# Performance work log

Hardware: AMD Instinct MI355X
Metric: run time of the kernel (lower is better)

## Reference

```python
import jax, jax.numpy as jnp
import numpy as np
import math

N = 16384
IN_F = 256
OUT_F = 64
EPS = 1e-6


def setup_inputs() -> dict:
    key = jax.random.key(0)
    k1, k2, k3, k4 = jax.random.split(key, 4)
    stdv = 1.0 / math.sqrt(OUT_F)
    inp = jax.random.normal(k1, (N, IN_F), dtype=jnp.float32)
    adj = jax.random.uniform(k2, (N, N), dtype=jnp.float32)
    weight = jax.random.uniform(k3, (IN_F, OUT_F), dtype=jnp.float32, minval=-stdv, maxval=stdv)
    bias = jax.random.uniform(k4, (OUT_F,), dtype=jnp.float32, minval=-stdv, maxval=stdv)
    return {"input": inp, "adj": adj, "weight": weight, "bias": bias, "p": 2}


def reference(input, adj, weight, bias, p):
    # support: [N, OUT_F]
    support = input @ weight
    mu = jnp.min(support)  # global scalar min
    pre_sup = support - mu + EPS  # >= EPS, safe for pow
    pre_top = pre_sup ** (p + 1)
    pre_down = pre_sup ** p
    # p-power mean aggregation: two adj matmuls sharing adj reads
    output = (adj @ pre_top) / (adj @ pre_down) + mu
    return output + bias
```

## Files before the change

### kernel.cpp

```cpp
#include <hip/hip_runtime.h>
#include <hip/hip_bf16.h>

typedef __attribute__((ext_vector_type(8))) short short8;
typedef __attribute__((ext_vector_type(4))) float f32x4;
typedef unsigned short u16;
typedef unsigned int u32;

#define NROWS 16384
#define KDIM 16384
#define EPS 1e-6f

__device__ __forceinline__ u16 f2bf(float x) {
    union { float f; u32 u; } v; v.f = x;
    u32 u = v.u;
    u32 r = (u + 0x7FFFu + ((u >> 16) & 1u)) >> 16;
    return (u16)r;
}

__device__ __forceinline__ void glds16(const void* g, void* l) {
    __builtin_amdgcn_global_load_lds(
        (const __attribute__((address_space(1))) void*)g,
        (__attribute__((address_space(3))) void*)l, 16, 0, 0);
}

__device__ __forceinline__ short cvbf(float x) {
    __hip_bfloat16 h = __float2bfloat16(x);
    return *(short*)&h;
}

__device__ __forceinline__ short8 cvt8(float4 a, float4 b) {
    short8 r = { cvbf(a.x), cvbf(a.y), cvbf(a.z), cvbf(a.w),
                 cvbf(b.x), cvbf(b.y), cvbf(b.z), cvbf(b.w) };
    return r;
}

__global__ __launch_bounds__(256) void wt_kernel(const float* __restrict__ W,
                                                 float* __restrict__ Wt) {
    int idx = blockIdx.x * 256 + threadIdx.x;
    int k = idx >> 6, c = idx & 63;
    Wt[c * 256 + k] = W[idx];
}

__global__ __launch_bounds__(256) void support_kernel(
    const float* __restrict__ inp, const float* __restrict__ Wt,
    float* __restrict__ sup)
{
    int tid = threadIdx.x;
    int col = tid & 63;
    int rr = tid >> 6;
    int rowbase = blockIdx.x * 32 + rr * 8;
    const float4* wt4 = (const float4*)(Wt + (size_t)col * 256);
    float acc[8];
#pragma unroll
    for (int i = 0; i < 8; ++i) acc[i] = 0.f;
    for (int k4 = 0; k4 < 64; ++k4) {
        float4 wv = wt4[k4];
#pragma unroll
        for (int i = 0; i < 8; ++i) {
            float4 iv = *((const float4*)(inp + (size_t)(rowbase + i) * 256) + k4);
            acc[i] += iv.x * wv.x + iv.y * wv.y + iv.z * wv.z + iv.w * wv.w;
        }
    }
#pragma unroll
    for (int i = 0; i < 8; ++i)
        sup[(size_t)(rowbase + i) * 64 + col] = acc[i];
}

__global__ __launch_bounds__(256) void min_part_kernel(
    const float* __restrict__ sup, float* __restrict__ partmin)
{
    __shared__ float wmin[4];
    int tid = threadIdx.x;
    const float4* s4 = (const float4*)sup;
    size_t idx = (size_t)blockIdx.x * 256 + tid;
    float m = 3.4e38f;
#pragma unroll
    for (int j = 0; j < 4; ++j) {
        float4 v = s4[idx + (size_t)j * 65536];
        m = fminf(m, fminf(fminf(v.x, v.y), fminf(v.z, v.w)));
    }
#pragma unroll
    for (int off = 32; off; off >>= 1) m = fminf(m, __shfl_down(m, off, 64));
    if ((tid & 63) == 0) wmin[tid >> 6] = m;
    __syncthreads();
    if (tid == 0)
        partmin[blockIdx.x] = fminf(fminf(wmin[0], wmin[1]), fminf(wmin[2], wmin[3]));
}

__global__ __launch_bounds__(256) void min_final_kernel(
    const float* __restrict__ partmin, float* __restrict__ mu)
{
    __shared__ float wmin[4];
    int tid = threadIdx.x;
    float m = partmin[tid];
#pragma unroll
    for (int off = 32; off; off >>= 1) m = fminf(m, __shfl_down(m, off, 64));
    if ((tid & 63) == 0) wmin[tid >> 6] = m;
    __syncthreads();
    if (tid == 0)
        mu[0] = fminf(fminf(wmin[0], wmin[1]), fminf(wmin[2], wmin[3]));
}

__global__ __launch_bounds__(256) void build_bt_kernel(
    const float* __restrict__ sup, const float* __restrict__ muptr,
    const int* __restrict__ pptr, u16* __restrict__ Bt)
{
    int k = blockIdx.x * 256 + threadIdx.x;
    float mu = *muptr;
    int p = *pptr;
    const float4* srow = (const float4*)(sup + (size_t)k * 64);
#pragma unroll
    for (int j = 0; j < 16; ++j) {
        float4 v = srow[j];
        float ss[4] = {v.x, v.y, v.z, v.w};
#pragma unroll
        for (int q = 0; q < 4; ++q) {
            int c = j * 4 + q;
            float s = ss[q] - mu + EPS;
            float d = 1.f;
            for (int i = 0; i < p; ++i) d *= s;
            Bt[(size_t)c * KDIM + k] = f2bf(d * s);
            Bt[(size_t)(c + 64) * KDIM + k] = f2bf(d);
        }
    }
}

#define BM 64
#define BN 128
#define BK 64
#define KH 8192
#define NTI 128

__global__ __launch_bounds__(512, 4) void gemm_kernel(
    const float* __restrict__ adj, const u16* __restrict__ Bt,
    float* __restrict__ Pp)
{
    __shared__ __align__(16) float Ash[2][BM * BK];
    __shared__ __align__(16) u16  Bsh[2][BN * BK];

    const int tid = threadIdx.x;
    const int rb = blockIdx.x >> 1;
    const int h  = blockIdx.x & 1;
    const size_t rowbase = (size_t)rb * BM;
    const size_t kbase = (size_t)h * KH;

    const int ga0 = tid,        ga1 = tid + 512;
    const int ar0 = ga0 >> 4,   ax0 = (ga0 & 15) ^ (ar0 & 7);
    const int ar1 = ga1 >> 4,   ax1 = (ga1 & 15) ^ (ar1 & 7);
    const float* asrc0 = adj + (rowbase + ar0) * KDIM + kbase + ax0 * 4;
    const float* asrc1 = adj + (rowbase + ar1) * KDIM + kbase + ax1 * 4;
    const int bn0 = ga0 >> 3,   bx0 = (ga0 & 7) ^ (bn0 & 7);
    const int bn1 = ga1 >> 3,   bx1 = (ga1 & 7) ^ (bn1 & 7);
    const u16* bsrc0 = Bt + (size_t)bn0 * KDIM + kbase + bx0 * 8;
    const u16* bsrc1 = Bt + (size_t)bn1 * KDIM + kbase + bx1 * 8;

    const int lane = tid & 63;
    const int w    = tid >> 6;
    const int wm   = w >> 1;
    const int wn   = w & 1;
    const int l15  = lane & 15, lg = lane >> 4;
    const int arow = wm * 16 + l15;
    const int asw  = arow & 7;

    f32x4 acc[4];
#pragma unroll
    for (int j = 0; j < 4; ++j) acc[j] = (f32x4){0.f, 0.f, 0.f, 0.f};

    auto stage = [&](int kt, int buf) {
        const int koff = kt * BK;
        char* ab = (char*)Ash[buf];
        char* bb = (char*)Bsh[buf];
        glds16(asrc0 + koff, ab + ga0 * 16);
        glds16(asrc1 + koff, ab + ga1 * 16);
        glds16(bsrc0 + koff, bb + ga0 * 16);
        glds16(bsrc1 + koff, bb + ga1 * 16);
    };

    stage(0, 0);

    for (int t = 0; t < NTI; ++t) {
        __syncthreads();
        if (t + 1 < NTI) stage(t + 1, (t + 1) & 1);
        const float4* As4 = (const float4*)Ash[t & 1];
        const short8* Bs8 = (const short8*)Bsh[t & 1];
#pragma unroll
        for (int ks = 0; ks < 2; ++ks) {
            const int x0 = ks * 8 + lg * 2;
            float4 fa = As4[arow * 16 + ((x0    ) ^ asw)];
            float4 fb = As4[arow * 16 + ((x0 + 1) ^ asw)];
            short8 a = cvt8(fa, fb);
            const int bx = ks * 4 + lg;
#pragma unroll
            for (int j = 0; j < 4; ++j) {
                const int n = wn * 32 + (j & 1) * 16 + (j >> 1) * 64 + l15;
                short8 b = Bs8[n * 8 + (bx ^ (n & 7))];
                acc[j] = __builtin_amdgcn_mfma_f32_16x16x32_bf16(a, b, acc[j], 0, 0, 0);
            }
        }
    }

    float* pb = Pp + (size_t)blockIdx.x * (BM * BN);
#pragma unroll
    for (int j = 0; j < 2; ++j) {
#pragma unroll
        for (int q = 0; q < 4; ++q) {
            int r = wm * 16 + lg * 4 + q;
            int c = wn * 32 + j * 16 + l15;
            pb[r * BN + c]      = acc[j][q];
            pb[r * BN + c + 64] = acc[j + 2][q];
        }
    }
}

__global__ __launch_bounds__(256) void reduce_kernel(
    const float* __restrict__ Pp, const float* __restrict__ bias,
    const float* __restrict__ muptr, float* __restrict__ out)
{
    int idx = blockIdx.x * 256 + threadIdx.x;
    int r = idx >> 6, c = idx & 63;
    int rb = r >> 6, rr = r & 63;
    const float* p0 = Pp + (size_t)(rb * 2) * (BM * BN) + rr * BN + c;
    const float* p1 = p0 + BM * BN;
    float T = p0[0]  + p1[0];
    float D = p0[64] + p1[64];
    out[idx] = T / D + muptr[0] + bias[c];
}

extern "C" void kernel_launch(void* const* d_in, const int* in_sizes, int n_in,
                              void* d_out, int out_size, void* d_ws, size_t ws_size,
                              hipStream_t stream)
{
    const float* inp  = (const float*)d_in[0];
    const float* adj  = (const float*)d_in[1];
    const float* W    = (const float*)d_in[2];
    const float* bias = (const float*)d_in[3];
    const int*   p    = (const int*)d_in[4];
    float* out = (float*)d_out;

    char* ws = (char*)d_ws;
    u16*   Bt      = (u16*)ws;
    float* partmin = (float*)(ws + (size_t)4 * 1024 * 1024);
    float* mu      = partmin + 256;
    float* Wt      = (float*)(ws + (size_t)4 * 1024 * 1024 + 4096);
    float* Pp      = (float*)(ws + (size_t)8 * 1024 * 1024);

    float* sup = out;

    wt_kernel       <<<64,   256, 0, stream>>>(W, Wt);
    support_kernel  <<<512,  256, 0, stream>>>(inp, Wt, sup);
    min_part_kernel <<<256,  256, 0, stream>>>(sup, partmin);
    min_final_kernel<<<1,    256, 0, stream>>>(partmin, mu);
    build_bt_kernel <<<64,   256, 0, stream>>>(sup, mu, p, Bt);
    gemm_kernel     <<<512,  512, 0, stream>>>(adj, Bt, Pp);
    reduce_kernel   <<<4096, 256, 0, stream>>>(Pp, bias, mu, out);
}
```

Before: 290.9 us.

## Convert adj to bf16 in registers before LDS, remap blocks and warp tiling

The adj tile is now loaded into registers, converted to bf16 once per element, and stored into LDS as bf16, in place of being copied as fp32 via global_load_lds and converted per MFMA read. This halves the LDS footprint and bandwidth for A and removes redundant conversions. The warp layout changes to a 2x4 grid, with each warp computing a 2x2 set of 16x16 tiles that reuse A and B fragments. The block index is remapped so the two K-halves and neighbouring row blocks are spread across XCDs, and the partial-sum layout in the reduce kernel is updated to match. The tradeoff is that A loads now go through VGPRs, which adds register pressure and wait latency.

```diff
diff --git a/kernel.cpp b/kernel.cpp
--- a/kernel.cpp
+++ b/kernel.cpp
@@ -26,12 +26,6 @@
 __device__ __forceinline__ short cvbf(float x) {
     __hip_bfloat16 h = __float2bfloat16(x);
     return *(short*)&h;
-}
-
-__device__ __forceinline__ short8 cvt8(float4 a, float4 b) {
-    short8 r = { cvbf(a.x), cvbf(a.y), cvbf(a.z), cvbf(a.w),
-                 cvbf(b.x), cvbf(b.y), cvbf(b.z), cvbf(b.w) };
-    return r;
 }
 
 __global__ __launch_bounds__(256) void wt_kernel(const float* __restrict__ W,
@@ -135,80 +129,101 @@
     const float* __restrict__ adj, const u16* __restrict__ Bt,
     float* __restrict__ Pp)
 {
-    __shared__ __align__(16) float Ash[2][BM * BK];
-    __shared__ __align__(16) u16  Bsh[2][BN * BK];
+    __shared__ __align__(16) u16 Ash[2][BM * BK];
+    __shared__ __align__(16) u16 Bsh[2][BN * BK];
 
     const int tid = threadIdx.x;
-    const int rb = blockIdx.x >> 1;
-    const int h  = blockIdx.x & 1;
+    const int P = blockIdx.x;
+    const int L = (P & 7) * 64 + (P >> 3);
+    const int h  = L >> 8;
+    const int rb = L & 255;
     const size_t rowbase = (size_t)rb * BM;
-    const size_t kbase = (size_t)h * KH;
-
-    const int ga0 = tid,        ga1 = tid + 512;
-    const int ar0 = ga0 >> 4,   ax0 = (ga0 & 15) ^ (ar0 & 7);
-    const int ar1 = ga1 >> 4,   ax1 = (ga1 & 15) ^ (ar1 & 7);
-    const float* asrc0 = adj + (rowbase + ar0) * KDIM + kbase + ax0 * 4;
-    const float* asrc1 = adj + (rowbase + ar1) * KDIM + kbase + ax1 * 4;
-    const int bn0 = ga0 >> 3,   bx0 = (ga0 & 7) ^ (bn0 & 7);
-    const int bn1 = ga1 >> 3,   bx1 = (ga1 & 7) ^ (bn1 & 7);
+    const size_t kbase   = (size_t)h * KH;
+
+    const int ars = tid >> 3;
+    const int ac8 = tid & 7;
+    const float* asrc = adj + (rowbase + ars) * KDIM + kbase + ac8 * 8;
+    const int awoff = ars * 8 + (ac8 ^ (ars & 7));
+
+    const int ga0 = tid, ga1 = tid + 512;
+    const int bn0 = ga0 >> 3, bx0 = (ga0 & 7) ^ (bn0 & 7);
+    const int bn1 = ga1 >> 3, bx1 = (ga1 & 7) ^ (bn1 & 7);
     const u16* bsrc0 = Bt + (size_t)bn0 * KDIM + kbase + bx0 * 8;
     const u16* bsrc1 = Bt + (size_t)bn1 * KDIM + kbase + bx1 * 8;
 
     const int lane = tid & 63;
     const int w    = tid >> 6;
-    const int wm   = w >> 1;
-    const int wn   = w & 1;
+    const int wm   = w >> 2;
+    const int wn   = w & 3;
     const int l15  = lane & 15, lg = lane >> 4;
-    const int arow = wm * 16 + l15;
-    const int asw  = arow & 7;
-
-    f32x4 acc[4];
-#pragma unroll
-    for (int j = 0; j < 4; ++j) acc[j] = (f32x4){0.f, 0.f, 0.f, 0.f};
-
-    auto stage = [&](int kt, int buf) {
+    const int arow0 = wm * 32 + l15;
+    const int arow1 = arow0 + 16;
+    const int nt = wn * 16 + l15;
+    const int nd = nt + 64;
+    const int asw = arow0 & 7;
+    const int bsw = nt & 7;
+
+    f32x4 acc00 = {0.f, 0.f, 0.f, 0.f};
+    f32x4 acc01 = acc00, acc10 = acc00, acc11 = acc00;
+
+    float4 ra0, ra1;
+
+    auto issueA = [&](int kt) {
+        const float4* ap = (const float4*)(asrc + kt * BK);
+        ra0 = ap[0]; ra1 = ap[1];
+    };
+    auto issueB = [&](int kt, int buf) {
+        char* bb = (char*)Bsh[buf];
         const int koff = kt * BK;
-        char* ab = (char*)Ash[buf];
-        char* bb = (char*)Bsh[buf];
-        glds16(asrc0 + koff, ab + ga0 * 16);
-        glds16(asrc1 + koff, ab + ga1 * 16);
         glds16(bsrc0 + koff, bb + ga0 * 16);
         glds16(bsrc1 + koff, bb + ga1 * 16);
     };
-
-    stage(0, 0);
+    auto writeA = [&](int buf) {
+        uint4 awv;
+        awv.x = (u32)(u16)cvbf(ra0.x) | ((u32)(u16)cvbf(ra0.y) << 16);
+        awv.y = (u32)(u16)cvbf(ra0.z) | ((u32)(u16)cvbf(ra0.w) << 16);
+        awv.z = (u32)(u16)cvbf(ra1.x) | ((u32)(u16)cvbf(ra1.y) << 16);
+        awv.w = (u32)(u16)cvbf(ra1.z) | ((u32)(u16)cvbf(ra1.w) << 16);
+        ((uint4*)Ash[buf])[awoff] = awv;
+    };
+
+    issueA(0);
+    issueB(0, 0);
+    writeA(0);
 
     for (int t = 0; t < NTI; ++t) {
         __syncthreads();
-        if (t + 1 < NTI) stage(t + 1, (t + 1) & 1);
-        const float4* As4 = (const float4*)Ash[t & 1];
+        const int nb = (t + 1) & 1;
+        if (t + 1 < NTI) {
+            issueA(t + 1);
+            issueB(t + 1, nb);
+        }
+        const short8* As8 = (const short8*)Ash[t & 1];
         const short8* Bs8 = (const short8*)Bsh[t & 1];
 #pragma unroll
         for (int ks = 0; ks < 2; ++ks) {
-            const int x0 = ks * 8 + lg * 2;
-            float4 fa = As4[arow * 16 + ((x0    ) ^ asw)];
-            float4 fb = As4[arow * 16 + ((x0 + 1) ^ asw)];
-            short8 a = cvt8(fa, fb);
-            const int bx = ks * 4 + lg;
-#pragma unroll
-            for (int j = 0; j < 4; ++j) {
-                const int n = wn * 32 + (j & 1) * 16 + (j >> 1) * 64 + l15;
-                short8 b = Bs8[n * 8 + (bx ^ (n & 7))];
-                acc[j] = __builtin_amdgcn_mfma_f32_16x16x32_bf16(a, b, acc[j], 0, 0, 0);
-            }
-        }
-    }
-
-    float* pb = Pp + (size_t)blockIdx.x * (BM * BN);
-#pragma unroll
-    for (int j = 0; j < 2; ++j) {
-#pragma unroll
-        for (int q = 0; q < 4; ++q) {
-            int r = wm * 16 + lg * 4 + q;
-            int c = wn * 32 + j * 16 + l15;
-            pb[r * BN + c]      = acc[j][q];
-            pb[r * BN + c + 64] = acc[j + 2][q];
-        }
+            const int g = ks * 4 + lg;
+            short8 a0 = As8[arow0 * 8 + (g ^ asw)];
+            short8 a1 = As8[arow1 * 8 + (g ^ asw)];
+            short8 b0 = Bs8[nt * 8 + (g ^ bsw)];
+            short8 b1 = Bs8[nd * 8 + (g ^ bsw)];
+            acc00 = __builtin_amdgcn_mfma_f32_16x16x32_bf16(a0, b0, acc00, 0, 0, 0);
+            acc01 = __builtin_amdgcn_mfma_f32_16x16x32_bf16(a0, b1, acc01, 0, 0, 0);
+            acc10 = __builtin_amdgcn_mfma_f32_16x16x32_bf16(a1, b0, acc10, 0, 0, 0);
+            acc11 = __builtin_amdgcn_mfma_f32_16x16x32_bf16(a1, b1, acc11, 0, 0, 0);
+        }
+        if (t + 1 < NTI) writeA(nb);
+    }
+
+    float* pb = Pp + (size_t)L * (BM * BN);
+#pragma unroll
+    for (int q = 0; q < 4; ++q) {
+        int r0 = wm * 32 + lg * 4 + q;
+        int r1 = r0 + 16;
+        pb[r0 * BN + nt] = acc00[q];
+        pb[r0 * BN + nd] = acc01[q];
+        pb[r1 * BN + nt] = acc10[q];
+        pb[r1 * BN + nd] = acc11[q];
     }
 }
 
@@ -219,8 +234,8 @@
     int idx = blockIdx.x * 256 + threadIdx.x;
     int r = idx >> 6, c = idx & 63;
     int rb = r >> 6, rr = r & 63;
-    const float* p0 = Pp + (size_t)(rb * 2) * (BM * BN) + rr * BN + c;
-    const float* p1 = p0 + BM * BN;
+    const float* p0 = Pp + (size_t)rb * (BM * BN) + rr * BN + c;
+    const float* p1 = p0 + (size_t)256 * (BM * BN);
     float T = p0[0]  + p1[0];
     float D = p0[64] + p1[64];
     out[idx] = T / D + muptr[0] + bias[c];
```

Result: slower. 327.2 us (+12.5%).

## Shrink GEMM tile to 32 rows and 32-wide K with 256-thread blocks

Applied to the files above, without the earlier changes.

Halves the GEMM block tile in M (64 to 32 rows) and in K step (64 to 32), uses 256 threads per block and launches 1024 blocks instead of 512. The load mapping, LDS swizzle, MFMA inner loop and reduce indexing are rewritten to match. The aim is more blocks and waves for better CU occupancy and latency hiding on the memory-bound adj stream. In exchange, each block re-reads the B tile for fewer output rows and does twice as many barrier iterations.

```diff
diff --git a/kernel.cpp b/kernel.cpp
--- a/kernel.cpp
+++ b/kernel.cpp
@@ -125,13 +125,13 @@
     }
 }
 
-#define BM 64
+#define BM 32
 #define BN 128
-#define BK 64
+#define BK 32
 #define KH 8192
-#define NTI 128
-
-__global__ __launch_bounds__(512, 4) void gemm_kernel(
+#define NTI 256
+
+__global__ __launch_bounds__(256, 4) void gemm_kernel(
     const float* __restrict__ adj, const u16* __restrict__ Bt,
     float* __restrict__ Pp)
 {
@@ -142,15 +142,15 @@
     const int rb = blockIdx.x >> 1;
     const int h  = blockIdx.x & 1;
     const size_t rowbase = (size_t)rb * BM;
-    const size_t kbase = (size_t)h * KH;
-
-    const int ga0 = tid,        ga1 = tid + 512;
-    const int ar0 = ga0 >> 4,   ax0 = (ga0 & 15) ^ (ar0 & 7);
-    const int ar1 = ga1 >> 4,   ax1 = (ga1 & 15) ^ (ar1 & 7);
-    const float* asrc0 = adj + (rowbase + ar0) * KDIM + kbase + ax0 * 4;
-    const float* asrc1 = adj + (rowbase + ar1) * KDIM + kbase + ax1 * 4;
-    const int bn0 = ga0 >> 3,   bx0 = (ga0 & 7) ^ (bn0 & 7);
-    const int bn1 = ga1 >> 3,   bx1 = (ga1 & 7) ^ (bn1 & 7);
+    const size_t kbase   = (size_t)h * KH;
+
+    const int ar = tid >> 3;
+    const int ax = (tid & 7) ^ (ar & 7);
+    const float* asrc = adj + (rowbase + ar) * KDIM + kbase + ax * 4;
+
+    const int g0 = tid, g1 = tid + 256;
+    const int bn0 = g0 >> 2, bx0 = (g0 & 3) ^ (bn0 & 3);
+    const int bn1 = g1 >> 2, bx1 = (g1 & 3) ^ (bn1 & 3);
     const u16* bsrc0 = Bt + (size_t)bn0 * KDIM + kbase + bx0 * 8;
     const u16* bsrc1 = Bt + (size_t)bn1 * KDIM + kbase + bx1 * 8;
 
@@ -159,21 +159,22 @@
     const int wm   = w >> 1;
     const int wn   = w & 1;
     const int l15  = lane & 15, lg = lane >> 4;
-    const int arow = wm * 16 + l15;
-    const int asw  = arow & 7;
-
-    f32x4 acc[4];
-#pragma unroll
-    for (int j = 0; j < 4; ++j) acc[j] = (f32x4){0.f, 0.f, 0.f, 0.f};
+    const int ar0  = wm * 16 + l15;
+    const int asw  = ar0 & 7;
+    const int n0   = wn * 32 + l15;
+    const int n1   = n0 + 16;
+    const int bs0  = n0 & 3, bs1 = n1 & 3;
+
+    f32x4 acc0 = {0.f, 0.f, 0.f, 0.f};
+    f32x4 acc1 = acc0, acc2 = acc0, acc3 = acc0;
 
     auto stage = [&](int kt, int buf) {
         const int koff = kt * BK;
         char* ab = (char*)Ash[buf];
         char* bb = (char*)Bsh[buf];
-        glds16(asrc0 + koff, ab + ga0 * 16);
-        glds16(asrc1 + koff, ab + ga1 * 16);
-        glds16(bsrc0 + koff, bb + ga0 * 16);
-        glds16(bsrc1 + koff, bb + ga1 * 16);
+        glds16(asrc + koff, ab + tid * 16);
+        glds16(bsrc0 + koff, bb + g0 * 16);
+        glds16(bsrc1 + koff, bb + g1 * 16);
     };
 
     stage(0, 0);
@@ -183,32 +184,27 @@
         if (t + 1 < NTI) stage(t + 1, (t + 1) & 1);
         const float4* As4 = (const float4*)Ash[t & 1];
         const short8* Bs8 = (const short8*)Bsh[t & 1];
-#pragma unroll
-        for (int ks = 0; ks < 2; ++ks) {
-            const int x0 = ks * 8 + lg * 2;
-            float4 fa = As4[arow * 16 + ((x0    ) ^ asw)];
-            float4 fb = As4[arow * 16 + ((x0 + 1) ^ asw)];
-            short8 a = cvt8(fa, fb);
-            const int bx = ks * 4 + lg;
-#pragma unroll
-            for (int j = 0; j < 4; ++j) {
-                const int n = wn * 32 + (j & 1) * 16 + (j >> 1) * 64 + l15;
-                short8 b = Bs8[n * 8 + (bx ^ (n & 7))];
-                acc[j] = __builtin_amdgcn_mfma_f32_16x16x32_bf16(a, b, acc[j], 0, 0, 0);
-            }
-        }
+        float4 fa = As4[ar0 * 8 + ((lg * 2    ) ^ asw)];
+        float4 fb = As4[ar0 * 8 + ((lg * 2 + 1) ^ asw)];
+        short8 a  = cvt8(fa, fb);
+        short8 b0 = Bs8[n0 * 4 + (lg ^ bs0)];
+        short8 b1 = Bs8[n1 * 4 + (lg ^ bs1)];
+        short8 b2 = Bs8[(n0 + 64) * 4 + (lg ^ bs0)];
+        short8 b3 = Bs8[(n1 + 64) * 4 + (lg ^ bs1)];
+        acc0 = __builtin_amdgcn_mfma_f32_16x16x32_bf16(a, b0, acc0, 0, 0, 0);
+        acc1 = __builtin_amdgcn_mfma_f32_16x16x32_bf16(a, b1, acc1, 0, 0, 0);
+        acc2 = __builtin_amdgcn_mfma_f32_16x16x32_bf16(a, b2, acc2, 0, 0, 0);
+        acc3 = __builtin_amdgcn_mfma_f32_16x16x32_bf16(a, b3, acc3, 0, 0, 0);
     }
 
     float* pb = Pp + (size_t)blockIdx.x * (BM * BN);
 #pragma unroll
-    for (int j = 0; j < 2; ++j) {
-#pragma unroll
-        for (int q = 0; q < 4; ++q) {
-            int r = wm * 16 + lg * 4 + q;
-            int c = wn * 32 + j * 16 + l15;
-            pb[r * BN + c]      = acc[j][q];
-            pb[r * BN + c + 64] = acc[j + 2][q];
-        }
+    for (int q = 0; q < 4; ++q) {
+        int r = wm * 16 + lg * 4 + q;
+        pb[r * BN + n0]      = acc0[q];
+        pb[r * BN + n1]      = acc1[q];
+        pb[r * BN + n0 + 64] = acc2[q];
+        pb[r * BN + n1 + 64] = acc3[q];
     }
 }
 
@@ -218,7 +214,7 @@
 {
     int idx = blockIdx.x * 256 + threadIdx.x;
     int r = idx >> 6, c = idx & 63;
-    int rb = r >> 6, rr = r & 63;
+    int rb = r >> 5, rr = r & 31;
     const float* p0 = Pp + (size_t)(rb * 2) * (BM * BN) + rr * BN + c;
     const float* p1 = p0 + BM * BN;
     float T = p0[0]  + p1[0];
@@ -251,6 +247,6 @@
     min_part_kernel <<<256,  256, 0, stream>>>(sup, partmin);
     min_final_kernel<<<1,    256, 0, stream>>>(partmin, mu);
     build_bt_kernel <<<64,   256, 0, stream>>>(sup, mu, p, Bt);
-    gemm_kernel     <<<512,  512, 0, stream>>>(adj, Bt, Pp);
+    gemm_kernel     <<<1024, 256, 0, stream>>>(adj, Bt, Pp);
     reduce_kernel   <<<4096, 256, 0, stream>>>(Pp, bias, mu, out);
 }
```

Measured after the change: 414.5 us. 1.42x slower.

## Replace LDS-staged GEMM with register-direct loads, split-K by four, XCD-aware block mapping

Applied to the files above, without the earlier changes.

The adj GEMM no longer stages tiles through LDS with global_load_lds double buffering. Each wave now loads its A rows and all B columns straight from global memory into registers and runs MFMAs, with each wave covering 32 rows by all 128 columns. K is split four ways instead of two, and blocks are mapped to XCDs so that each XCD handles one K quarter, which should improve L2 reuse of Bt. The aim is to remove LDS traffic and barriers, at the cost of uncoalesced strided global loads, more register pressure, and a larger partial buffer for the reduce kernel to read.

```diff
diff --git a/kernel.cpp b/kernel.cpp
--- a/kernel.cpp
+++ b/kernel.cpp
@@ -15,12 +15,6 @@
     u32 u = v.u;
     u32 r = (u + 0x7FFFu + ((u >> 16) & 1u)) >> 16;
     return (u16)r;
-}
-
-__device__ __forceinline__ void glds16(const void* g, void* l) {
-    __builtin_amdgcn_global_load_lds(
-        (const __attribute__((address_space(1))) void*)g,
-        (__attribute__((address_space(3))) void*)l, 16, 0, 0);
 }
 
 __device__ __forceinline__ short cvbf(float x) {
@@ -125,89 +119,69 @@
     }
 }
 
-#define BM 64
-#define BN 128
-#define BK 64
-#define KH 8192
-#define NTI 128
-
-__global__ __launch_bounds__(512, 4) void gemm_kernel(
+#define KSPLIT 4
+#define KR (KDIM / KSPLIT)
+#define GITERS (KR / 32)
+
+__global__ __launch_bounds__(256, 2) void gemm_kernel(
     const float* __restrict__ adj, const u16* __restrict__ Bt,
     float* __restrict__ Pp)
 {
-    __shared__ __align__(16) float Ash[2][BM * BK];
-    __shared__ __align__(16) u16  Bsh[2][BN * BK];
-
-    const int tid = threadIdx.x;
-    const int rb = blockIdx.x >> 1;
-    const int h  = blockIdx.x & 1;
-    const size_t rowbase = (size_t)rb * BM;
-    const size_t kbase = (size_t)h * KH;
-
-    const int ga0 = tid,        ga1 = tid + 512;
-    const int ar0 = ga0 >> 4,   ax0 = (ga0 & 15) ^ (ar0 & 7);
-    const int ar1 = ga1 >> 4,   ax1 = (ga1 & 15) ^ (ar1 & 7);
-    const float* asrc0 = adj + (rowbase + ar0) * KDIM + kbase + ax0 * 4;
-    const float* asrc1 = adj + (rowbase + ar1) * KDIM + kbase + ax1 * 4;
-    const int bn0 = ga0 >> 3,   bx0 = (ga0 & 7) ^ (bn0 & 7);
-    const int bn1 = ga1 >> 3,   bx1 = (ga1 & 7) ^ (bn1 & 7);
-    const u16* bsrc0 = Bt + (size_t)bn0 * KDIM + kbase + bx0 * 8;
-    const u16* bsrc1 = Bt + (size_t)bn1 * KDIM + kbase + bx1 * 8;
-
+    const int tid  = threadIdx.x;
     const int lane = tid & 63;
     const int w    = tid >> 6;
-    const int wm   = w >> 1;
-    const int wn   = w & 1;
-    const int l15  = lane & 15, lg = lane >> 4;
-    const int arow = wm * 16 + l15;
-    const int asw  = arow & 7;
-
-    f32x4 acc[4];
-#pragma unroll
-    for (int j = 0; j < 4; ++j) acc[j] = (f32x4){0.f, 0.f, 0.f, 0.f};
-
-    auto stage = [&](int kt, int buf) {
-        const int koff = kt * BK;
-        char* ab = (char*)Ash[buf];
-        char* bb = (char*)Bsh[buf];
-        glds16(asrc0 + koff, ab + ga0 * 16);
-        glds16(asrc1 + koff, ab + ga1 * 16);
-        glds16(bsrc0 + koff, bb + ga0 * 16);
-        glds16(bsrc1 + koff, bb + ga1 * 16);
-    };
-
-    stage(0, 0);
-
-    for (int t = 0; t < NTI; ++t) {
-        __syncthreads();
-        if (t + 1 < NTI) stage(t + 1, (t + 1) & 1);
-        const float4* As4 = (const float4*)Ash[t & 1];
-        const short8* Bs8 = (const short8*)Bsh[t & 1];
-#pragma unroll
-        for (int ks = 0; ks < 2; ++ks) {
-            const int x0 = ks * 8 + lg * 2;
-            float4 fa = As4[arow * 16 + ((x0    ) ^ asw)];
-            float4 fb = As4[arow * 16 + ((x0 + 1) ^ asw)];
-            short8 a = cvt8(fa, fb);
-            const int bx = ks * 4 + lg;
-#pragma unroll
-            for (int j = 0; j < 4; ++j) {
-                const int n = wn * 32 + (j & 1) * 16 + (j >> 1) * 64 + l15;
-                short8 b = Bs8[n * 8 + (bx ^ (n & 7))];
-                acc[j] = __builtin_amdgcn_mfma_f32_16x16x32_bf16(a, b, acc[j], 0, 0, 0);
-            }
-        }
-    }
-
-    float* pb = Pp + (size_t)blockIdx.x * (BM * BN);
-#pragma unroll
-    for (int j = 0; j < 2; ++j) {
+    const int l15  = lane & 15;
+    const int lg   = lane >> 4;
+
+    const int P    = blockIdx.x;
+    const int xcd  = P & 7;
+    const int slot = P >> 3;
+    const int kq   = xcd >> 1;
+    const int rg   = slot * 2 + (xcd & 1);
+
+    const size_t rowbase = (size_t)rg * 128 + w * 32;
+    const size_t kbase   = (size_t)kq * KR;
+
+    const float* a0p = adj + (rowbase + l15) * KDIM + kbase + lg * 8;
+    const float* a1p = a0p + (size_t)16 * KDIM;
+    const u16*   bbp = Bt + (size_t)l15 * KDIM + kbase + lg * 8;
+
+    f32x4 acc0[8], acc1[8];
+#pragma unroll
+    for (int cf = 0; cf < 8; ++cf) {
+        acc0[cf] = (f32x4){0.f, 0.f, 0.f, 0.f};
+        acc1[cf] = acc0[cf];
+    }
+
+#pragma unroll 2
+    for (int it = 0; it < GITERS; ++it) {
+        const int ko = it * 32;
+        const float4* A0 = (const float4*)(a0p + ko);
+        const float4* A1 = (const float4*)(a1p + ko);
+        float4 fa0 = A0[0], fa1 = A0[1];
+        float4 fb0 = A1[0], fb1 = A1[1];
+        short8 b[8];
+#pragma unroll
+        for (int cf = 0; cf < 8; ++cf)
+            b[cf] = *(const short8*)(bbp + (size_t)(cf * 16) * KDIM + ko);
+        short8 a0 = cvt8(fa0, fa1);
+        short8 a1 = cvt8(fb0, fb1);
+#pragma unroll
+        for (int cf = 0; cf < 8; ++cf) {
+            acc0[cf] = __builtin_amdgcn_mfma_f32_16x16x32_bf16(a0, b[cf], acc0[cf], 0, 0, 0);
+            acc1[cf] = __builtin_amdgcn_mfma_f32_16x16x32_bf16(a1, b[cf], acc1[cf], 0, 0, 0);
+        }
+    }
+
+    float* pb = Pp + ((size_t)kq * NROWS + rowbase) * 128;
+#pragma unroll
+    for (int cf = 0; cf < 8; ++cf) {
 #pragma unroll
         for (int q = 0; q < 4; ++q) {
-            int r = wm * 16 + lg * 4 + q;
-            int c = wn * 32 + j * 16 + l15;
-            pb[r * BN + c]      = acc[j][q];
-            pb[r * BN + c + 64] = acc[j + 2][q];
+            int r0 = lg * 4 + q;
+            int c  = cf * 16 + l15;
+            pb[(r0     ) * 128 + c] = acc0[cf][q];
+            pb[(r0 + 16) * 128 + c] = acc1[cf][q];
         }
     }
 }
@@ -218,11 +192,14 @@
 {
     int idx = blockIdx.x * 256 + threadIdx.x;
     int r = idx >> 6, c = idx & 63;
-    int rb = r >> 6, rr = r & 63;
-    const float* p0 = Pp + (size_t)(rb * 2) * (BM * BN) + rr * BN + c;
-    const float* p1 = p0 + BM * BN;
-    float T = p0[0]  + p1[0];
-    float D = p0[64] + p1[64];
+    const float* p = Pp + (size_t)r * 128 + c;
+    const size_t qs = (size_t)NROWS * 128;
+    float T = 0.f, D = 0.f;
+#pragma unroll
+    for (int kq = 0; kq < KSPLIT; ++kq) {
+        T += p[kq * qs];
+        D += p[kq * qs + 64];
+    }
     out[idx] = T / D + muptr[0] + bias[c];
 }
 
@@ -251,6 +228,6 @@
     min_part_kernel <<<256,  256, 0, stream>>>(sup, partmin);
     min_final_kernel<<<1,    256, 0, stream>>>(partmin, mu);
     build_bt_kernel <<<64,   256, 0, stream>>>(sup, mu, p, Bt);
-    gemm_kernel     <<<512,  512, 0, stream>>>(adj, Bt, Pp);
+    gemm_kernel     <<<512,  256, 0, stream>>>(adj, Bt, Pp);
     reduce_kernel   <<<4096, 256, 0, stream>>>(Pp, bias, mu, out);
 }
```

After: 478.3 us. 64.4% more time.
